# Kernel tuning notes

Hardware: AMD Instinct MI355X
Metric: run time of the kernel (lower is better)

Reference implementation:

```python
import jax, jax.numpy as jnp
import numpy as np
from jax import lax

# pywt db4 decomposition filters (hardcoded to avoid pywt dependency)
DB4_DEC_LO = np.array([-0.010597401784997278, 0.032883011666982945,
                       0.030841381835986965, -0.18703481171888114,
                       -0.02798376941698385, 0.6308807679295904,
                       0.7148465705525415, 0.23037781330885523], dtype=np.float32)
DB4_DEC_HI = np.array([-0.23037781330885523, 0.7148465705525415,
                       -0.6308807679295904, -0.02798376941698385,
                       0.18703481171888114, 0.030841381835986965,
                       -0.032883011666982945, -0.010597401784997278], dtype=np.float32)

B, T, C = 32, 16384, 64

def setup_inputs() -> dict:
    key = jax.random.key(0)
    x = jax.random.normal(key, (B, T, C), dtype=jnp.float32)
    return {"x": x,
            "dec_lo": jnp.asarray(DB4_DEC_LO),
            "dec_hi": jnp.asarray(DB4_DEC_HI)}

def _depthwise_conv1d(xp, filt, channels):
    # xp: [B, L, C]; filt: [K]; depthwise stride-2 valid cross-correlation
    k = jnp.broadcast_to(filt[:, None, None], (filt.shape[0], 1, channels))  # [K,1,C]
    return lax.conv_general_dilated(
        xp, k, window_strides=(2,), padding='VALID',
        dimension_numbers=('NWC', 'WIO', 'NWC'),
        feature_group_count=channels)

def reference(x, dec_lo, dec_hi):
    channels = x.shape[-1]
    filter_length = dec_lo.shape[0]          # 8 for db4
    pad = filter_length - 1                   # 7
    crop = pad // 2                           # 3
    xp = jnp.pad(x, ((0, 0), (pad, pad), (0, 0)), mode='reflect')
    approx = _depthwise_conv1d(xp, dec_lo, channels)[:, crop:-crop, :]
    detail = _depthwise_conv1d(xp, dec_hi, channels)[:, crop:-crop, :]
    # original concatenates all approx channels then all detail channels
    return jnp.concatenate([approx, detail], axis=-1)  # [B, T/2-2, 2C]
```

## Files before the change

kernel.cpp:

```cpp
#include <hip/hip_runtime.h>


#define BT     32
#define TT     16384
#define CC     64
#define T2     8190
#define OC     128
#define TBLK   32
#define NROWS  72
#define NCHUNK 18

__global__ __launch_bounds__(256, 8) void dwt_db4_lds32_kernel(
    const float* __restrict__ x,
    const float* __restrict__ dec_lo,
    const float* __restrict__ dec_hi,
    float* __restrict__ out)
{
    __shared__ float lds[NROWS * CC];

    const int tid = threadIdx.x;
    const int b   = blockIdx.y;
    const int t0  = blockIdx.x * TBLK;
    const int row_base = (t0 == 0) ? 0 : (2 * t0 - 1);

    const float* __restrict__ xb = x + (size_t)b * TT * CC;

    {
        const int wave = tid >> 6;
        const int lane = tid & 63;
        const float* gsrc = xb + (size_t)row_base * CC + lane * 4;
        const float* gend = xb + (size_t)TT * CC - 4;
        #pragma unroll
        for (int j = 0; j < 5; ++j) {
            const int c = wave + j * 4;
            if (c < NCHUNK) {
                const float* g = gsrc + c * 256;
                g = (g > gend) ? gend : g;
                __builtin_amdgcn_global_load_lds(
                    (const __attribute__((address_space(1))) unsigned int*)g,
                    (__attribute__((address_space(3))) unsigned int*)&lds[c * 256],
                    16, 0, 0);
            }
        }
    }

    float flo[8], fhi[8];
    #pragma unroll
    for (int k = 0; k < 8; ++k) { flo[k] = dec_lo[k]; fhi[k] = dec_hi[k]; }

    __syncthreads();

    const int cg = tid & 15;
    const int sl = tid >> 4;
    const int t  = t0 + sl * 2;
    const int c4 = cg * 4;

    float4 w[10];
    #pragma unroll
    for (int i = 0; i < 10; ++i) {
        int m  = 2 * t - 1 + i;
        int mm = m < 0 ? -m : m;
        mm     = mm > (TT - 1) ? 2 * (TT - 1) - mm : mm;
        w[i] = *reinterpret_cast<const float4*>(&lds[(mm - row_base) * CC + c4]);
    }

    float4 alo0, ahi0, alo1, ahi1;
    alo0.x = alo0.y = alo0.z = alo0.w = 0.0f;
    ahi0.x = ahi0.y = ahi0.z = ahi0.w = 0.0f;
    alo1.x = alo1.y = alo1.z = alo1.w = 0.0f;
    ahi1.x = ahi1.y = ahi1.z = ahi1.w = 0.0f;

    #pragma unroll
    for (int k = 0; k < 8; ++k) {
        const float4 v0 = w[k];
        const float4 v1 = w[k + 2];
        alo0.x = fmaf(flo[k], v0.x, alo0.x);
        alo0.y = fmaf(flo[k], v0.y, alo0.y);
        alo0.z = fmaf(flo[k], v0.z, alo0.z);
        alo0.w = fmaf(flo[k], v0.w, alo0.w);
        ahi0.x = fmaf(fhi[k], v0.x, ahi0.x);
        ahi0.y = fmaf(fhi[k], v0.y, ahi0.y);
        ahi0.z = fmaf(fhi[k], v0.z, ahi0.z);
        ahi0.w = fmaf(fhi[k], v0.w, ahi0.w);

        alo1.x = fmaf(flo[k], v1.x, alo1.x);
        alo1.y = fmaf(flo[k], v1.y, alo1.y);
        alo1.z = fmaf(flo[k], v1.z, alo1.z);
        alo1.w = fmaf(flo[k], v1.w, alo1.w);
        ahi1.x = fmaf(fhi[k], v1.x, ahi1.x);
        ahi1.y = fmaf(fhi[k], v1.y, ahi1.y);
        ahi1.z = fmaf(fhi[k], v1.z, ahi1.z);
        ahi1.w = fmaf(fhi[k], v1.w, ahi1.w);
    }

    float* __restrict__ ob = out + (size_t)b * T2 * OC + (size_t)t * OC + c4;
    if (t < T2) {
        *reinterpret_cast<float4*>(ob)      = alo0;
        *reinterpret_cast<float4*>(ob + CC) = ahi0;
    }
    if (t + 1 < T2) {
        *reinterpret_cast<float4*>(ob + OC)      = alo1;
        *reinterpret_cast<float4*>(ob + OC + CC) = ahi1;
    }
}

extern "C" void kernel_launch(void* const* d_in, const int* in_sizes, int n_in,
                              void* d_out, int out_size, void* d_ws, size_t ws_size,
                              hipStream_t stream)
{
    const float* x      = (const float*)d_in[0];
    const float* dec_lo = (const float*)d_in[1];
    const float* dec_hi = (const float*)d_in[2];
    float*       out    = (float*)d_out;

    dim3 block(256);
    dim3 grid((T2 + TBLK - 1) / TBLK, BT);

    hipLaunchKernelGGL(dwt_db4_lds32_kernel, grid, block, 0, stream,
                       x, dec_lo, dec_hi, out);
}
```

Measured before the change: 232.8 us.

## Make DWT kernel persistent with double-buffered LDS prefetch across tiles

Turns the one-tile-per-block launch into a fixed grid of 1024 blocks, each walking 8 consecutive tiles. The input for the next tile is staged into a second LDS buffer with async global-to-LDS loads while the current tile is convolved and stored. The aim is to hide global load latency behind compute and to cut per-block launch overhead. In exchange it doubles LDS per block and lowers launch_bounds occupancy to 4. The barrier at the end of each iteration probably drains all outstanding memory ops, which may limit the overlap.

```diff
diff --git a/kernel.cpp b/kernel.cpp
--- a/kernel.cpp
+++ b/kernel.cpp
@@ -1,106 +1,125 @@
 #include <hip/hip_runtime.h>
 
 
-#define BT     32
-#define TT     16384
-#define CC     64
-#define T2     8190
-#define OC     128
-#define TBLK   32
-#define NROWS  72
-#define NCHUNK 18
+#define BT      32
+#define TT      16384
+#define CC      64
+#define T2      8190
+#define OC      128
+#define TBLK    32
+#define NROWS   72
+#define NCHUNK  18
+#define NTILE_T 256
+#define TPB     8
+#define NBLK    1024
 
-__global__ __launch_bounds__(256, 8) void dwt_db4_lds32_kernel(
+__global__ __launch_bounds__(256, 4) void dwt_db4_pipe_kernel(
     const float* __restrict__ x,
     const float* __restrict__ dec_lo,
     const float* __restrict__ dec_hi,
     float* __restrict__ out)
 {
-    __shared__ float lds[NROWS * CC];
+    __shared__ float lds[2][NROWS * CC];
 
-    const int tid = threadIdx.x;
-    const int b   = blockIdx.y;
-    const int t0  = blockIdx.x * TBLK;
-    const int row_base = (t0 == 0) ? 0 : (2 * t0 - 1);
-
-    const float* __restrict__ xb = x + (size_t)b * TT * CC;
-
-    {
-        const int wave = tid >> 6;
-        const int lane = tid & 63;
-        const float* gsrc = xb + (size_t)row_base * CC + lane * 4;
-        const float* gend = xb + (size_t)TT * CC - 4;
-        #pragma unroll
-        for (int j = 0; j < 5; ++j) {
-            const int c = wave + j * 4;
-            if (c < NCHUNK) {
-                const float* g = gsrc + c * 256;
-                g = (g > gend) ? gend : g;
-                __builtin_amdgcn_global_load_lds(
-                    (const __attribute__((address_space(1))) unsigned int*)g,
-                    (__attribute__((address_space(3))) unsigned int*)&lds[c * 256],
-                    16, 0, 0);
-            }
-        }
-    }
+    const int tid  = threadIdx.x;
+    const int wave = tid >> 6;
+    const int lane = tid & 63;
+    const int cg   = tid & 15;
+    const int sl   = tid >> 4;
+    const int c4   = cg * 4;
+    const int g0   = blockIdx.x * TPB;
 
     float flo[8], fhi[8];
     #pragma unroll
     for (int k = 0; k < 8; ++k) { flo[k] = dec_lo[k]; fhi[k] = dec_hi[k]; }
 
+    auto stage = [&](int g, float* dst) {
+        const int b        = g >> 8;
+        const int t0       = (g & 255) * TBLK;
+        const int row_base = (t0 == 0) ? 0 : (2 * t0 - 1);
+        const float* xb    = x + (size_t)b * TT * CC;
+        const float* gsrc  = xb + (size_t)row_base * CC + lane * 4;
+        const float* gend  = xb + (size_t)TT * CC - 4;
+        #pragma unroll
+        for (int j = 0; j < 5; ++j) {
+            const int c = wave + j * 4;
+            if (c < NCHUNK) {
+                const float* gp = gsrc + c * 256;
+                gp = (gp > gend) ? gend : gp;
+                __builtin_amdgcn_global_load_lds(
+                    (const __attribute__((address_space(1))) unsigned int*)gp,
+                    (__attribute__((address_space(3))) unsigned int*)&dst[c * 256],
+                    16, 0, 0);
+            }
+        }
+    };
+
+    auto compute = [&](int g, const float* buf) {
+        const int b        = g >> 8;
+        const int t0       = (g & 255) * TBLK;
+        const int row_base = (t0 == 0) ? 0 : (2 * t0 - 1);
+        const int t        = t0 + sl * 2;
+
+        float4 w[10];
+        #pragma unroll
+        for (int i = 0; i < 10; ++i) {
+            int m  = 2 * t - 1 + i;
+            int mm = m < 0 ? -m : m;
+            mm     = mm > (TT - 1) ? 2 * (TT - 1) - mm : mm;
+            w[i] = *reinterpret_cast<const float4*>(&buf[(mm - row_base) * CC + c4]);
+        }
+
+        float4 alo0, ahi0, alo1, ahi1;
+        alo0.x = alo0.y = alo0.z = alo0.w = 0.0f;
+        ahi0.x = ahi0.y = ahi0.z = ahi0.w = 0.0f;
+        alo1.x = alo1.y = alo1.z = alo1.w = 0.0f;
+        ahi1.x = ahi1.y = ahi1.z = ahi1.w = 0.0f;
+
+        #pragma unroll
+        for (int k = 0; k < 8; ++k) {
+            const float4 v0 = w[k];
+            const float4 v1 = w[k + 2];
+            alo0.x = fmaf(flo[k], v0.x, alo0.x);
+            alo0.y = fmaf(flo[k], v0.y, alo0.y);
+            alo0.z = fmaf(flo[k], v0.z, alo0.z);
+            alo0.w = fmaf(flo[k], v0.w, alo0.w);
+            ahi0.x = fmaf(fhi[k], v0.x, ahi0.x);
+            ahi0.y = fmaf(fhi[k], v0.y, ahi0.y);
+            ahi0.z = fmaf(fhi[k], v0.z, ahi0.z);
+            ahi0.w = fmaf(fhi[k], v0.w, ahi0.w);
+
+            alo1.x = fmaf(flo[k], v1.x, alo1.x);
+            alo1.y = fmaf(flo[k], v1.y, alo1.y);
+            alo1.z = fmaf(flo[k], v1.z, alo1.z);
+            alo1.w = fmaf(flo[k], v1.w, alo1.w);
+            ahi1.x = fmaf(fhi[k], v1.x, ahi1.x);
+            ahi1.y = fmaf(fhi[k], v1.y, ahi1.y);
+            ahi1.z = fmaf(fhi[k], v1.z, ahi1.z);
+            ahi1.w = fmaf(fhi[k], v1.w, ahi1.w);
+        }
+
+        float* ob = out + (size_t)b * T2 * OC + (size_t)t * OC + c4;
+        if (t < T2) {
+            *reinterpret_cast<float4*>(ob)      = alo0;
+            *reinterpret_cast<float4*>(ob + CC) = ahi0;
+        }
+        if (t + 1 < T2) {
+            *reinterpret_cast<float4*>(ob + OC)      = alo1;
+            *reinterpret_cast<float4*>(ob + OC + CC) = ahi1;
+        }
+    };
+
+    stage(g0, lds[0]);
     __syncthreads();
 
-    const int cg = tid & 15;
-    const int sl = tid >> 4;
-    const int t  = t0 + sl * 2;
-    const int c4 = cg * 4;
-
-    float4 w[10];
-    #pragma unroll
-    for (int i = 0; i < 10; ++i) {
-        int m  = 2 * t - 1 + i;
-        int mm = m < 0 ? -m : m;
-        mm     = mm > (TT - 1) ? 2 * (TT - 1) - mm : mm;
-        w[i] = *reinterpret_cast<const float4*>(&lds[(mm - row_base) * CC + c4]);
-    }
-
-    float4 alo0, ahi0, alo1, ahi1;
-    alo0.x = alo0.y = alo0.z = alo0.w = 0.0f;
-    ahi0.x = ahi0.y = ahi0.z = ahi0.w = 0.0f;
-    alo1.x = alo1.y = alo1.z = alo1.w = 0.0f;
-    ahi1.x = ahi1.y = ahi1.z = ahi1.w = 0.0f;
-
-    #pragma unroll
-    for (int k = 0; k < 8; ++k) {
-        const float4 v0 = w[k];
-        const float4 v1 = w[k + 2];
-        alo0.x = fmaf(flo[k], v0.x, alo0.x);
-        alo0.y = fmaf(flo[k], v0.y, alo0.y);
-        alo0.z = fmaf(flo[k], v0.z, alo0.z);
-        alo0.w = fmaf(flo[k], v0.w, alo0.w);
-        ahi0.x = fmaf(fhi[k], v0.x, ahi0.x);
-        ahi0.y = fmaf(fhi[k], v0.y, ahi0.y);
-        ahi0.z = fmaf(fhi[k], v0.z, ahi0.z);
-        ahi0.w = fmaf(fhi[k], v0.w, ahi0.w);
-
-        alo1.x = fmaf(flo[k], v1.x, alo1.x);
-        alo1.y = fmaf(flo[k], v1.y, alo1.y);
-        alo1.z = fmaf(flo[k], v1.z, alo1.z);
-        alo1.w = fmaf(flo[k], v1.w, alo1.w);
-        ahi1.x = fmaf(fhi[k], v1.x, ahi1.x);
-        ahi1.y = fmaf(fhi[k], v1.y, ahi1.y);
-        ahi1.z = fmaf(fhi[k], v1.z, ahi1.z);
-        ahi1.w = fmaf(fhi[k], v1.w, ahi1.w);
-    }
-
-    float* __restrict__ ob = out + (size_t)b * T2 * OC + (size_t)t * OC + c4;
-    if (t < T2) {
-        *reinterpret_cast<float4*>(ob)      = alo0;
-        *reinterpret_cast<float4*>(ob + CC) = ahi0;
-    }
-    if (t + 1 < T2) {
-        *reinterpret_cast<float4*>(ob + OC)      = alo1;
-        *reinterpret_cast<float4*>(ob + OC + CC) = ahi1;
+    #pragma unroll 2
+    for (int i = 0; i < TPB; ++i) {
+        const int cur = i & 1;
+        if (i + 1 < TPB)
+            stage(g0 + i + 1, lds[cur ^ 1]);
+        __builtin_amdgcn_sched_barrier(0);
+        compute(g0 + i, lds[cur]);
+        __syncthreads();
     }
 }
 
@@ -114,8 +133,8 @@
     float*       out    = (float*)d_out;
 
     dim3 block(256);
-    dim3 grid((T2 + TBLK - 1) / TBLK, BT);
+    dim3 grid(NBLK);
 
-    hipLaunchKernelGGL(dwt_db4_lds32_kernel, grid, block, 0, stream,
+    hipLaunchKernelGGL(dwt_db4_pipe_kernel, grid, block, 0, stream,
                        x, dec_lo, dec_hi, out);
 }
```

After: 244.2 us. 4.9% more time.
